# Kernel tuning notes

Measured on AMD Instinct MI355X. Metric: run time of the kernel, lower is better.

## Reference

```python
import jax, jax.numpy as jnp
import numpy as np

B, T, C = 2, 2048, 1024
H = 16
D = C // H  # head_dim = 64


def setup_inputs() -> dict:
    key = jax.random.key(0)
    k1, k2, k3, k4, k5 = jax.random.split(key, 5)
    s = 1.0 / np.sqrt(C)
    return {
        "x": jax.random.normal(k1, (B, T, C), dtype=jnp.float32),
        "w_qkv": jax.random.normal(k2, (C, 3 * C), dtype=jnp.float32) * s,
        "b_qkv": jax.random.normal(k3, (3 * C,), dtype=jnp.float32) * 0.01,
        "w_out": jax.random.normal(k4, (C, C), dtype=jnp.float32) * s,
        "b_out": jax.random.normal(k5, (C,), dtype=jnp.float32) * 0.01,
    }


def reference(x, w_qkv, b_qkv, w_out, b_out):
    Bx, Tx, Cx = x.shape
    qkv = x @ w_qkv + b_qkv                      # [B,T,3C]
    qkv = qkv.reshape(Bx, Tx, 3, H, D)
    q, k, v = qkv[:, :, 0], qkv[:, :, 1], qkv[:, :, 2]  # [B,T,H,D]
    # [B,H,T,T] scores with scaling
    scores = jnp.einsum("bqhd,bkhd->bhqk", q, k) / np.sqrt(D).astype(np.float32)
    causal = jnp.tril(jnp.ones((Tx, Tx), dtype=bool))
    scores = jnp.where(causal[None, None], scores, -jnp.inf)
    attn = jax.nn.softmax(scores, axis=-1)
    out = jnp.einsum("bhqk,bkhd->bqhd", attn, v).reshape(Bx, Tx, Cx)
    return out @ w_out + b_out
```

## Files before the change

### kernel.cpp

```cpp
#include <hip/hip_runtime.h>
#include <stdint.h>

typedef unsigned short u16;
typedef __attribute__((ext_vector_type(8))) short bfrag;
typedef __attribute__((ext_vector_type(4))) short bfrag4;
typedef __attribute__((ext_vector_type(4))) float f32x4;

#define MFMA_BF16 __builtin_amdgcn_mfma_f32_16x16x32_bf16

static constexpr int Bc = 2;
static constexpr int Tc = 2048;
static constexpr int Cc = 1024;
static constexpr int Hc = 16;
static constexpr int Dc = 64;
static constexpr int N3 = 3 * Cc;

__device__ __forceinline__ u16 f2bf(float f) {
    union { unsigned int i; float f; } v; v.f = f;
    unsigned int u = v.i;
    u += 0x7fffu + ((u >> 16) & 1u);
    return (u16)(u >> 16);
}
__device__ __forceinline__ unsigned int fbits(float f) {
    union { unsigned int i; float f; } v; v.f = f; return v.i;
}
__device__ __forceinline__ unsigned int pack_bf2(float hi, float lo) {
    return __builtin_amdgcn_perm(fbits(hi), fbits(lo), 0x07060302u);
}

#if __has_builtin(__builtin_amdgcn_mfma_f32_16x16x16bf16_1k)
__device__ __forceinline__ f32x4 MFMA16(bfrag4 a, bfrag4 b, f32x4 c) {
    return __builtin_amdgcn_mfma_f32_16x16x16bf16_1k(a, b, c, 0, 0, 0);
}
#elif __has_builtin(__builtin_amdgcn_mfma_f32_16x16x16_bf16)
__device__ __forceinline__ f32x4 MFMA16(bfrag4 a, bfrag4 b, f32x4 c) {
    return __builtin_amdgcn_mfma_f32_16x16x16_bf16(a, b, c, 0, 0, 0);
}
#else
__device__ __forceinline__ f32x4 MFMA16(bfrag4 a, bfrag4 b, f32x4 c) {
    bfrag a8 = {a[0], a[1], a[2], a[3], 0, 0, 0, 0};
    bfrag b8 = {b[0], b[1], b[2], b[3], 0, 0, 0, 0};
    return MFMA_BF16(a8, b8, c, 0, 0, 0);
}
#endif

__device__ __forceinline__ void async_load16(const u16* g, u16* lds) {
    __builtin_amdgcn_global_load_lds(
        (const __attribute__((address_space(1))) unsigned int*)g,
        (__attribute__((address_space(3))) unsigned int*)lds, 16, 0, 0);
}

__global__ __launch_bounds__(256) void prep(
    const float* __restrict__ x, const float* __restrict__ w_qkv,
    const float* __restrict__ w_out, u16* __restrict__ xb,
    u16* __restrict__ WqkvT, u16* __restrict__ WoutT) {
    __shared__ u16 tile[32][33];
    const int blk = blockIdx.x, tid = threadIdx.x;
    if (blk < 4096) {
        const int i = (blk * 256 + tid) * 4;
        const float4 v = *(const float4*)(x + i);
        ushort4 o;
        o.x = f2bf(v.x); o.y = f2bf(v.y); o.z = f2bf(v.z); o.w = f2bf(v.w);
        *(ushort4*)(xb + i) = o;
        return;
    }
    const float* in; u16* out; int rows, cols, c0, r0;
    if (blk < 4096 + 3072) {
        const int t = blk - 4096;
        in = w_qkv; out = WqkvT; rows = 1024; cols = 3072;
        c0 = (t % 96) * 32; r0 = (t / 96) * 32;
    } else {
        const int t = blk - 7168;
        in = w_out; out = WoutT; rows = 1024; cols = 1024;
        c0 = (t & 31) * 32; r0 = (t >> 5) * 32;
    }
    const int row = tid >> 3;
    const int cg  = (tid & 7) * 4;
    const float4 v = *(const float4*)(in + (size_t)(r0 + row) * cols + c0 + cg);
    tile[cg + 0][row] = f2bf(v.x);
    tile[cg + 1][row] = f2bf(v.y);
    tile[cg + 2][row] = f2bf(v.z);
    tile[cg + 3][row] = f2bf(v.w);
    __syncthreads();
    const int tx = tid & 31, ty = tid >> 5;
    for (int i = 0; i < 4; i++)
        out[(size_t)(c0 + ty + 8 * i) * rows + r0 + tx] = tile[ty + 8 * i][tx];
}

__global__ __launch_bounds__(512, 2) void gemm_qkv(
    const u16* __restrict__ A, const u16* __restrict__ BT,
    const float* __restrict__ bias, u16* __restrict__ outQK,
    u16* __restrict__ Vt, int M, int Nn, int K) {
    extern __shared__ __align__(16) u16 smem[];
    u16* As = smem;
    u16* Bs = smem + 3 * (128 * 32);

    const int tid  = threadIdx.x;
    const int wave = tid >> 6, lane = tid & 63;
    const int quad = lane >> 4, l16 = lane & 15;
    const int wm = wave >> 2, wn = wave & 3;
    const int m0 = blockIdx.y * 128, n0 = blockIdx.x * 384;

    f32x4 acc[4][6];
    #pragma unroll
    for (int i = 0; i < 4; i++)
        #pragma unroll
        for (int j = 0; j < 6; j++)
            acc[i][j] = (f32x4){0.f, 0.f, 0.f, 0.f};

    const int rA = lane >> 2;
    const int cA = ((lane & 3) ^ (rA & 3)) * 8;

    const u16* Ag  = A  + (size_t)(m0 + wave * 16 + rA) * K + cA;
    const u16* Bg0 = BT + (size_t)(n0 + wave * 48 + rA) * K + cA;
    u16* ldsA = As + (wave * 16) * 32;
    u16* ldsB = Bs + (wave * 48) * 32;

    const int swz8 = (quad ^ (l16 & 3)) * 8;
    int offA[4], offB[6];
    #pragma unroll
    for (int mt = 0; mt < 4; mt++)
        offA[mt] = (wm * 64 + mt * 16 + l16) * 32 + swz8;
    #pragma unroll
    for (int nt = 0; nt < 6; nt++)
        offB[nt] = (wn * 96 + nt * 16 + l16) * 32 + swz8;

    #define STAGE_Q(t, bsel)                                                   \
        {                                                                      \
            const int k0_ = (t) << 5;                                          \
            async_load16(Ag + k0_, ldsA + (bsel) * (128 * 32));                \
            _Pragma("unroll")                                                  \
            for (int j = 0; j < 3; j++)                                        \
                async_load16(Bg0 + (size_t)(j * 16) * K + k0_,                 \
                             ldsB + (bsel) * (384 * 32) + j * (16 * 32));      \
        }

    STAGE_Q(0, 0);
    STAGE_Q(1, 1);

    const int T = K >> 5;
    for (int t = 0; t < T; t++) {
        if (t + 1 < T) asm volatile("s_waitcnt vmcnt(4)" ::: "memory");
        else           asm volatile("s_waitcnt vmcnt(0)" ::: "memory");
        __builtin_amdgcn_s_barrier();
        asm volatile("" ::: "memory");
        if (t + 2 < T) { STAGE_Q(t + 2, (t + 2) % 3); }

        const u16* Ab = As + (t % 3) * (128 * 32);
        const u16* Bb = Bs + (t % 3) * (384 * 32);
        bfrag af[4], bf[6];
        #pragma unroll
        for (int mt = 0; mt < 4; mt++) af[mt] = *(const bfrag*)(Ab + offA[mt]);
        #pragma unroll
        for (int nt = 0; nt < 6; nt++) bf[nt] = *(const bfrag*)(Bb + offB[nt]);

        __builtin_amdgcn_s_setprio(1);
        #pragma unroll
        for (int mt = 0; mt < 4; mt++)
            #pragma unroll
            for (int nt = 0; nt < 6; nt++)
                acc[mt][nt] = MFMA_BF16(af[mt], bf[nt], acc[mt][nt], 0, 0, 0);
        __builtin_amdgcn_s_setprio(0);
    }
    #undef STAGE_Q

    #pragma unroll
    for (int nt = 0; nt < 6; nt++) {
        const int gn = n0 + wn * 96 + nt * 16 + l16;
        const float bv = bias[gn];
        if (gn < 2 * Cc) {
            const float scl = (gn < Cc) ? 0.125f : 1.0f;
            #pragma unroll
            for (int mt = 0; mt < 4; mt++) {
                #pragma unroll
                for (int r = 0; r < 4; r++) {
                    const int gm = m0 + wm * 64 + mt * 16 + quad * 4 + r;
                    outQK[(size_t)gm * Nn + gn] = f2bf((acc[mt][nt][r] + bv) * scl);
                }
            }
        } else {
            const int gnv = gn - 2 * Cc;
            const int h = gnv >> 6, d = gnv & 63;
            #pragma unroll
            for (int mt = 0; mt < 4; mt++) {
                const int gmb = m0 + wm * 64 + mt * 16 + quad * 4;
                const int b = gmb >> 11, trow = gmb & (Tc - 1);
                ushort4 o;
                o.x = f2bf(acc[mt][nt][0] + bv);
                o.y = f2bf(acc[mt][nt][1] + bv);
                o.z = f2bf(acc[mt][nt][2] + bv);
                o.w = f2bf(acc[mt][nt][3] + bv);
                *(ushort4*)(Vt + ((size_t)((b * Hc + h) * Dc + d)) * Tc + trow) = o;
            }
        }
    }
}

__global__ __launch_bounds__(512, 2) void gemm_out(
    const u16* __restrict__ A, const u16* __restrict__ BT,
    const float* __restrict__ bias, float* __restrict__ out,
    int M, int Nn, int K) {
    extern __shared__ __align__(16) u16 smem[];
    u16* As = smem;
    u16* Bs = smem + 3 * (128 * 32);

    const int tid  = threadIdx.x;
    const int wave = tid >> 6, lane = tid & 63;
    const int quad = lane >> 4, l16 = lane & 15;
    const int wm = wave >> 2, wn = wave & 3;
    const int m0 = blockIdx.y * 128, n0 = blockIdx.x * 128;

    f32x4 acc[4][2];
    #pragma unroll
    for (int i = 0; i < 4; i++)
        #pragma unroll
        for (int j = 0; j < 2; j++)
            acc[i][j] = (f32x4){0.f, 0.f, 0.f, 0.f};

    const int rA = lane >> 2;
    const int cA = ((lane & 3) ^ (rA & 3)) * 8;

    const u16* Ag = A  + (size_t)(m0 + wave * 16 + rA) * K + cA;
    const u16* Bg = BT + (size_t)(n0 + wave * 16 + rA) * K + cA;
    u16* ldsA = As + (wave * 16) * 32;
    u16* ldsB = Bs + (wave * 16) * 32;

    const int swz8 = (quad ^ (l16 & 3)) * 8;
    int offA[4], offB[2];
    #pragma unroll
    for (int mt = 0; mt < 4; mt++)
        offA[mt] = (wm * 64 + mt * 16 + l16) * 32 + swz8;
    #pragma unroll
    for (int nt = 0; nt < 2; nt++)
        offB[nt] = (wn * 32 + nt * 16 + l16) * 32 + swz8;

    #define STAGE_O(t, bsel)                                                   \
        {                                                                      \
            const int k0_ = (t) << 5;                                          \
            async_load16(Ag + k0_, ldsA + (bsel) * (128 * 32));                \
            async_load16(Bg + k0_, ldsB + (bsel) * (128 * 32));                \
        }

    STAGE_O(0, 0);
    STAGE_O(1, 1);

    const int T = K >> 5;
    for (int t = 0; t < T; t++) {
        if (t + 1 < T) asm volatile("s_waitcnt vmcnt(2)" ::: "memory");
        else           asm volatile("s_waitcnt vmcnt(0)" ::: "memory");
        __builtin_amdgcn_s_barrier();
        asm volatile("" ::: "memory");
        if (t + 2 < T) { STAGE_O(t + 2, (t + 2) % 3); }

        const u16* Ab = As + (t % 3) * (128 * 32);
        const u16* Bb = Bs + (t % 3) * (128 * 32);
        bfrag af[4], bf[2];
        #pragma unroll
        for (int mt = 0; mt < 4; mt++) af[mt] = *(const bfrag*)(Ab + offA[mt]);
        #pragma unroll
        for (int nt = 0; nt < 2; nt++) bf[nt] = *(const bfrag*)(Bb + offB[nt]);

        __builtin_amdgcn_s_setprio(1);
        #pragma unroll
        for (int mt = 0; mt < 4; mt++)
            #pragma unroll
            for (int nt = 0; nt < 2; nt++)
                acc[mt][nt] = MFMA_BF16(af[mt], bf[nt], acc[mt][nt], 0, 0, 0);
        __builtin_amdgcn_s_setprio(0);
    }
    #undef STAGE_O

    #pragma unroll
    for (int nt = 0; nt < 2; nt++) {
        const int gn = n0 + wn * 32 + nt * 16 + l16;
        const float bv = bias[gn];
        #pragma unroll
        for (int mt = 0; mt < 4; mt++) {
            #pragma unroll
            for (int r = 0; r < 4; r++) {
                const int gm = m0 + wm * 64 + mt * 16 + quad * 4 + r;
                out[(size_t)gm * Nn + gn] = acc[mt][nt][r] + bv;
            }
        }
    }
}

__global__ __launch_bounds__(256, 4) void attn_kernel(
    const u16* __restrict__ QKVp, const u16* __restrict__ Vt,
    u16* __restrict__ Ob) {
    __shared__ __align__(16) u16 KsF[2][64 * 64];
    __shared__ __align__(16) u16 VsF[2][64 * 64];

    const int tid  = threadIdx.x;
    const int wave = tid >> 6, lane = tid & 63;
    const int quad = lane >> 4, l16 = lane & 15;

    const int bh = blockIdx.x & 31;
    const int g5 = blockIdx.x >> 5;
    const int jq = (g5 < 8) ? 31 - g5
                 : (g5 < 16) ? g5 + 8
                 : (g5 < 24) ? 31 - g5
                 : g5 - 24;
    const int b = bh >> 4, h = bh & 15;
    const u16* Qp = QKVp + (size_t)b * Tc * N3 + h * Dc;
    const u16* Kp = Qp + Cc;
    const u16* Vp = Vt + (size_t)bh * Dc * Tc;

    const int qw = jq * 64 + wave * 16;

    const int row8 = lane >> 3;
    const int swz  = ((lane & 7) ^ row8) * 8;
    const int pk0 = ((quad)     ^ (l16 & 7)) * 8;
    const int pk1 = ((quad + 4) ^ (l16 & 7)) * 8;

    bfrag qf0, qf1;
    {
        const u16* qp = Qp + (size_t)(qw + l16) * N3 + quad * 8;
        qf0 = *(const bfrag*)qp;
        qf1 = *(const bfrag*)(qp + 32);
    }

    float l_i = 0.f;
    f32x4 oacc[4];
    #pragma unroll
    for (int g = 0; g < 4; g++) oacc[g] = (f32x4){0.f, 0.f, 0.f, 0.f};

    #define STAGEKV(t, bsel)                                                    \
        {                                                                       \
            const int k0_ = (t) * 64;                                           \
            _Pragma("unroll")                                                   \
            for (int j = 0; j < 2; j++) {                                       \
                const int rr = wave * 16 + j * 8;                               \
                const int gr = rr + row8;                                       \
                async_load16(Kp + (size_t)(k0_ + gr) * N3 + swz,                \
                             &KsF[bsel][rr * 64]);                              \
                async_load16(Vp + (size_t)gr * Tc + k0_ + swz,                  \
                             &VsF[bsel][rr * 64]);                              \
            }                                                                   \
        }

    STAGEKV(0, 0);
    for (int t = 0; t <= jq; t++) {
        __syncthreads();
        if (t < jq) STAGEKV(t + 1, (t + 1) & 1);
        const u16* Kb = KsF[t & 1];
        const u16* Vb = VsF[t & 1];

        f32x4 s[4];
        __builtin_amdgcn_s_setprio(1);
        #pragma unroll
        for (int g = 0; g < 4; g++) {
            const u16* kb = Kb + (g * 16 + l16) * 64;
            bfrag kf0 = *(const bfrag*)(kb + pk0);
            bfrag kf1 = *(const bfrag*)(kb + pk1);
            f32x4 z = (f32x4){0.f, 0.f, 0.f, 0.f};
            z = MFMA_BF16(kf0, qf0, z, 0, 0, 0);
            z = MFMA_BF16(kf1, qf1, z, 0, 0, 0);
            s[g] = z;
        }
        __builtin_amdgcn_s_setprio(0);

        #pragma unroll
        for (int g = 0; g < 4; g++)
            #pragma unroll
            for (int r = 0; r < 4; r++)
                s[g][r] = __expf(s[g][r]);
        if (t == jq) {
            #pragma unroll
            for (int g = 0; g < 4; g++)
                #pragma unroll
                for (int r = 0; r < 4; r++)
                    if (g * 16 + quad * 4 + r > wave * 16 + l16) s[g][r] = 0.f;
        }
        #pragma unroll
        for (int g = 0; g < 4; g++)
            l_i += s[g][0] + s[g][1] + s[g][2] + s[g][3];

        __builtin_amdgcn_s_setprio(1);
        #pragma unroll
        for (int g = 0; g < 4; g++) {
            union { unsigned int u[2]; bfrag4 v; } pf;
            pf.u[0] = pack_bf2(s[g][1], s[g][0]);
            pf.u[1] = pack_bf2(s[g][3], s[g][2]);
            const int vc = ((2 * g + (quad >> 1)) ^ (l16 & 7)) * 8 + (quad & 1) * 4;
            #pragma unroll
            for (int ng = 0; ng < 4; ng++) {
                const bfrag4 vf = *(const bfrag4*)(Vb + (ng * 16 + l16) * 64 + vc);
                oacc[ng] = MFMA16(vf, pf.v, oacc[ng]);
            }
        }
        __builtin_amdgcn_s_setprio(0);
    }
    #undef STAGEKV

    float rs = l_i;
    rs += __shfl_xor(rs, 16);
    rs += __shfl_xor(rs, 32);
    const float inv = 1.f / rs;
    const int q = qw + l16;
    u16* orow = Ob + (size_t)(b * Tc + q) * Cc + h * Dc + quad * 4;
    #pragma unroll
    for (int ng = 0; ng < 4; ng++) {
        ushort4 o;
        o.x = f2bf(oacc[ng][0] * inv);
        o.y = f2bf(oacc[ng][1] * inv);
        o.z = f2bf(oacc[ng][2] * inv);
        o.w = f2bf(oacc[ng][3] * inv);
        *(ushort4*)(orow + ng * 16) = o;
    }
}

extern "C" void kernel_launch(void* const* d_in, const int* in_sizes, int n_in,
                              void* d_out, int out_size, void* d_ws, size_t ws_size,
                              hipStream_t stream) {
    const float* x     = (const float*)d_in[0];
    const float* w_qkv = (const float*)d_in[1];
    const float* b_qkv = (const float*)d_in[2];
    const float* w_out = (const float*)d_in[3];
    const float* b_out = (const float*)d_in[4];
    float* out = (float*)d_out;
    u16* ws  = (u16*)d_ws;

    u16* xb    = ws;
    u16* WqkvT = xb    + (size_t)4096 * 1024;
    u16* WoutT = WqkvT + (size_t)3072 * 1024;
    u16* QKVp  = WoutT + (size_t)1024 * 1024;
    u16* Vt    = QKVp  + (size_t)4096 * 3072;
    u16* Ao    = xb;

    static bool smem_set = false;
    if (!smem_set) {
        hipFuncSetAttribute(reinterpret_cast<const void*>(gemm_qkv),
                            hipFuncAttributeMaxDynamicSharedMemorySize,
                            96 * 1024);
        hipFuncSetAttribute(reinterpret_cast<const void*>(gemm_out),
                            hipFuncAttributeMaxDynamicSharedMemorySize,
                            48 * 1024);
        smem_set = true;
    }

    prep<<<8192, 256, 0, stream>>>(x, w_qkv, w_out, xb, WqkvT, WoutT);
    gemm_qkv<<<dim3(3072 / 384, 4096 / 128), 512, 96 * 1024, stream>>>(
        xb, WqkvT, b_qkv, QKVp, Vt, 4096, 3072, 1024);
    attn_kernel<<<1024, 256, 0, stream>>>(QKVp, Vt, Ao);
    gemm_out<<<dim3(1024 / 128, 4096 / 128), 512, 48 * 1024, stream>>>(
        Ao, WoutT, b_out, out, 4096, 1024, 1024);
}
```

Before: 175.2 us.

## Deepen QKV GEMM pipeline to four stages and split MFMA phases

Reworks the QKV projection GEMM main loop to use a four-buffer LDS ring with a prefetch depth of three K-steps. Each iteration is split into two half-N MFMA phases, and global loads for future tiles are interleaved between them with explicit barriers, waitcnts and sched_barriers. The LDS swizzle changes to pack row pairs into 64-element lines, and the problem dimensions become compile-time constants. The goal is to hide global-load latency and LDS bank conflicts better. In exchange the dynamic LDS request grows to 128 KB and each iteration carries more barriers.

```diff
diff --git a/kernel.cpp b/kernel.cpp
--- a/kernel.cpp
+++ b/kernel.cpp
@@ -90,10 +90,11 @@
 __global__ __launch_bounds__(512, 2) void gemm_qkv(
     const u16* __restrict__ A, const u16* __restrict__ BT,
     const float* __restrict__ bias, u16* __restrict__ outQK,
-    u16* __restrict__ Vt, int M, int Nn, int K) {
+    u16* __restrict__ Vt) {
+    constexpr int Kd = 1024, Nn = 3072, Td = 32;
     extern __shared__ __align__(16) u16 smem[];
     u16* As = smem;
-    u16* Bs = smem + 3 * (128 * 32);
+    u16* Bs = smem + 4 * (128 * 32);
 
     const int tid  = threadIdx.x;
     const int wave = tid >> 6, lane = tid & 63;
@@ -108,61 +109,91 @@
         for (int j = 0; j < 6; j++)
             acc[i][j] = (f32x4){0.f, 0.f, 0.f, 0.f};
 
-    const int rA = lane >> 2;
-    const int cA = ((lane & 3) ^ (rA & 3)) * 8;
-
-    const u16* Ag  = A  + (size_t)(m0 + wave * 16 + rA) * K + cA;
-    const u16* Bg0 = BT + (size_t)(n0 + wave * 48 + rA) * K + cA;
+    const int rloc = 2 * (lane >> 3) + ((lane >> 2) & 1);
+    const int cg   = ((lane & 3) ^ ((lane >> 3) & 3)) * 8;
+    const int rk   = (l16 >> 1) & 3;
+    const int rodd = (l16 & 1) * 32;
+
+    const u16* Ag = A  + (size_t)(m0 + wave * 16 + rloc) * Kd + cg;
+    const u16* Bg = BT + (size_t)(n0 + wave * 48 + rloc) * Kd + cg;
     u16* ldsA = As + (wave * 16) * 32;
     u16* ldsB = Bs + (wave * 48) * 32;
 
-    const int swz8 = (quad ^ (l16 & 3)) * 8;
     int offA[4], offB[6];
     #pragma unroll
-    for (int mt = 0; mt < 4; mt++)
-        offA[mt] = (wm * 64 + mt * 16 + l16) * 32 + swz8;
-    #pragma unroll
-    for (int nt = 0; nt < 6; nt++)
-        offB[nt] = (wn * 96 + nt * 16 + l16) * 32 + swz8;
-
-    #define STAGE_Q(t, bsel)                                                   \
-        {                                                                      \
-            const int k0_ = (t) << 5;                                          \
-            async_load16(Ag + k0_, ldsA + (bsel) * (128 * 32));                \
-            _Pragma("unroll")                                                  \
-            for (int j = 0; j < 3; j++)                                        \
-                async_load16(Bg0 + (size_t)(j * 16) * K + k0_,                 \
-                             ldsB + (bsel) * (384 * 32) + j * (16 * 32));      \
-        }
-
-    STAGE_Q(0, 0);
-    STAGE_Q(1, 1);
-
-    const int T = K >> 5;
-    for (int t = 0; t < T; t++) {
-        if (t + 1 < T) asm volatile("s_waitcnt vmcnt(4)" ::: "memory");
-        else           asm volatile("s_waitcnt vmcnt(0)" ::: "memory");
+    for (int mt = 0; mt < 4; mt++) {
+        const int r = wm * 64 + mt * 16 + l16;
+        offA[mt] = (r >> 1) * 64 + rodd + (quad ^ rk) * 8;
+    }
+    #pragma unroll
+    for (int nt = 0; nt < 6; nt++) {
+        const int r = wn * 96 + nt * 16 + l16;
+        offB[nt] = (r >> 1) * 64 + rodd + (quad ^ rk) * 8;
+    }
+
+    #define GLD_A(h, bsel)                                                     \
+        async_load16(Ag + ((h) << 5), ldsA + (bsel) * (128 * 32));
+    #define GLD_B(h, bsel, j)                                                  \
+        async_load16(Bg + (size_t)((j) * 16) * Kd + ((h) << 5),                \
+                     ldsB + (bsel) * (384 * 32) + (j) * (16 * 32));
+
+    #pragma unroll
+    for (int h = 0; h < 3; h++) {
+        GLD_A(h, h);
+        GLD_B(h, h, 0); GLD_B(h, h, 1); GLD_B(h, h, 2);
+    }
+    asm volatile("s_waitcnt vmcnt(8)" ::: "memory");
+    __builtin_amdgcn_s_barrier();
+    asm volatile("" ::: "memory");
+
+    for (int h = 0; h < Td; h++) {
+        const int bsel = h & 3;
+        const u16* Ab = As + bsel * (128 * 32);
+        const u16* Bb = Bs + bsel * (384 * 32);
+        const int psel = (h + 3) & 3;
+
+        bfrag af[4], bf0[3];
+        #pragma unroll
+        for (int mt = 0; mt < 4; mt++) af[mt] = *(const bfrag*)(Ab + offA[mt]);
+        #pragma unroll
+        for (int nt = 0; nt < 3; nt++) bf0[nt] = *(const bfrag*)(Bb + offB[nt]);
+        if (h + 3 < Td) { GLD_A(h + 3, psel); GLD_B(h + 3, psel, 0); }
+        __builtin_amdgcn_s_barrier();
+        asm volatile("s_waitcnt lgkmcnt(0)" ::: "memory");
+        __builtin_amdgcn_sched_barrier(0);
+        __builtin_amdgcn_s_setprio(1);
+        #pragma unroll
+        for (int mt = 0; mt < 4; mt++)
+            #pragma unroll
+            for (int nt = 0; nt < 3; nt++)
+                acc[mt][nt] = MFMA_BF16(af[mt], bf0[nt], acc[mt][nt], 0, 0, 0);
+        __builtin_amdgcn_s_setprio(0);
         __builtin_amdgcn_s_barrier();
         asm volatile("" ::: "memory");
-        if (t + 2 < T) { STAGE_Q(t + 2, (t + 2) % 3); }
-
-        const u16* Ab = As + (t % 3) * (128 * 32);
-        const u16* Bb = Bs + (t % 3) * (384 * 32);
-        bfrag af[4], bf[6];
-        #pragma unroll
-        for (int mt = 0; mt < 4; mt++) af[mt] = *(const bfrag*)(Ab + offA[mt]);
-        #pragma unroll
-        for (int nt = 0; nt < 6; nt++) bf[nt] = *(const bfrag*)(Bb + offB[nt]);
-
+
+        bfrag bf1[3];
+        #pragma unroll
+        for (int nt = 0; nt < 3; nt++)
+            bf1[nt] = *(const bfrag*)(Bb + offB[nt + 3]);
+        if (h + 3 < Td) { GLD_B(h + 3, psel, 1); GLD_B(h + 3, psel, 2); }
+        if (h <= Td - 4)      asm volatile("s_waitcnt vmcnt(8)" ::: "memory");
+        else if (h == Td - 3) asm volatile("s_waitcnt vmcnt(4)" ::: "memory");
+        else if (h == Td - 2) asm volatile("s_waitcnt vmcnt(0)" ::: "memory");
+        __builtin_amdgcn_s_barrier();
+        asm volatile("s_waitcnt lgkmcnt(0)" ::: "memory");
+        __builtin_amdgcn_sched_barrier(0);
         __builtin_amdgcn_s_setprio(1);
         #pragma unroll
         for (int mt = 0; mt < 4; mt++)
             #pragma unroll
-            for (int nt = 0; nt < 6; nt++)
-                acc[mt][nt] = MFMA_BF16(af[mt], bf[nt], acc[mt][nt], 0, 0, 0);
+            for (int nt = 0; nt < 3; nt++)
+                acc[mt][nt + 3] = MFMA_BF16(af[mt], bf1[nt], acc[mt][nt + 3], 0, 0, 0);
         __builtin_amdgcn_s_setprio(0);
-    }
-    #undef STAGE_Q
+        __builtin_amdgcn_s_barrier();
+        asm volatile("" ::: "memory");
+    }
+    #undef GLD_A
+    #undef GLD_B
 
     #pragma unroll
     for (int nt = 0; nt < 6; nt++) {
@@ -432,7 +463,7 @@
     if (!smem_set) {
         hipFuncSetAttribute(reinterpret_cast<const void*>(gemm_qkv),
                             hipFuncAttributeMaxDynamicSharedMemorySize,
-                            96 * 1024);
+                            128 * 1024);
         hipFuncSetAttribute(reinterpret_cast<const void*>(gemm_out),
                             hipFuncAttributeMaxDynamicSharedMemorySize,
                             48 * 1024);
@@ -440,8 +471,8 @@
     }
 
     prep<<<8192, 256, 0, stream>>>(x, w_qkv, w_out, xb, WqkvT, WoutT);
-    gemm_qkv<<<dim3(3072 / 384, 4096 / 128), 512, 96 * 1024, stream>>>(
-        xb, WqkvT, b_qkv, QKVp, Vt, 4096, 3072, 1024);
+    gemm_qkv<<<dim3(3072 / 384, 4096 / 128), 512, 128 * 1024, stream>>>(
+        xb, WqkvT, b_qkv, QKVp, Vt);
     attn_kernel<<<1024, 256, 0, stream>>>(QKVp, Vt, Ao);
     gemm_out<<<dim3(1024 / 128, 4096 / 128), 512, 48 * 1024, stream>>>(
         Ao, WoutT, b_out, out, 4096, 1024, 1024);
```

Measured after the change: 173.7 us. No clear change (-0.8%).
